# Kernel tuning notes

Measured on AMD Instinct MI355X. Metric: run time of the kernel, lower is better.

## Reference

```python
import jax, jax.numpy as jnp
import numpy as np

NUM_HEADS = 16
D_MODEL = 1024
D_K = D_MODEL // NUM_HEADS
B, S = 2, 2048


def setup_inputs() -> dict:
    key = jax.random.key(0)
    ks = jax.random.split(key, 10)
    q = jax.random.normal(ks[0], (B, S, D_MODEL), dtype=jnp.float32)
    k = jax.random.normal(ks[1], (B, S, D_MODEL), dtype=jnp.float32)
    v = jax.random.normal(ks[2], (B, S, D_MODEL), dtype=jnp.float32)
    # causal mask, 1 = keep, 0 = masked (masked_fill(mask==0, -1e9))
    mask = jnp.tril(jnp.ones((S, S), dtype=jnp.int32))[None, None, :, :]
    # Linear weights ~ N(0, 0.02); biases left at torch default-ish small uniform
    std = 0.02
    Wq = jax.random.normal(ks[3], (D_MODEL, D_MODEL), dtype=jnp.float32) * std
    Wk = jax.random.normal(ks[4], (D_MODEL, D_MODEL), dtype=jnp.float32) * std
    Wv = jax.random.normal(ks[5], (D_MODEL, D_MODEL), dtype=jnp.float32) * std
    bound = 1.0 / np.sqrt(D_MODEL)
    bq = jax.random.uniform(ks[6], (D_MODEL,), jnp.float32, -bound, bound)
    bk = jax.random.uniform(ks[7], (D_MODEL,), jnp.float32, -bound, bound)
    bv = jax.random.uniform(ks[8], (D_MODEL,), jnp.float32, -bound, bound)
    return {"q": q, "k": k, "v": v, "mask": mask,
            "Wq": Wq, "bq": bq, "Wk": Wk, "bk": bk, "Wv": Wv, "bv": bv}


def reference(q, k, v, mask, Wq, bq, Wk, bk, Wv, bv):
    # projections (torch Linear: x @ W.T + b), split heads -> [B, H, S, Dk]
    def proj(x, W, b):
        y = x @ W.T + b
        return y.reshape(B, S, NUM_HEADS, D_K).transpose(0, 2, 1, 3)

    qh, kh, vh = proj(q, Wq, bq), proj(k, Wk, bk), proj(v, Wv, bv)
    scores = jnp.einsum('bhqd,bhkd->bhqk', qh, kh) / jnp.sqrt(jnp.float32(D_K))
    scores = jnp.where(mask == 0, jnp.float32(-1e9), scores)
    p = jax.nn.softmax(scores, axis=-1)
    # dropout is identity in eval mode
    x = jnp.einsum('bhqk,bhkd->bhqd', p, vh)  # [B, H, S, Dk]
    return x.transpose(0, 2, 1, 3).reshape(B, S, D_MODEL)
```

## Files before the change

kernel.cpp:

```cpp
#include <hip/hip_runtime.h>

#define B_ 2
#define H_ 16
#define S_ 2048
#define DM 1024
#define DK 64
#define NX (4096 * 1024)
#define NW (1024 * 1024)

typedef unsigned short u16;
typedef __attribute__((ext_vector_type(8))) short bf16x8;
typedef __attribute__((ext_vector_type(8))) unsigned short u16x8;
typedef __attribute__((ext_vector_type(4))) unsigned short u16x4;
typedef __attribute__((ext_vector_type(4))) float f32x4;

__device__ inline u16 f2bf(float f) {
  union { float f; unsigned int u; } c; c.f = f;
  unsigned int u = c.u;
  u += 0x7fffu + ((u >> 16) & 1u);
  return (u16)(u >> 16);
}

__device__ inline u16x8 cvt8(const float* __restrict__ src) {
  const float4 a = *reinterpret_cast<const float4*>(src);
  const float4 b = *reinterpret_cast<const float4*>(src + 4);
  u16x8 r;
  r[0] = f2bf(a.x); r[1] = f2bf(a.y); r[2] = f2bf(a.z); r[3] = f2bf(a.w);
  r[4] = f2bf(b.x); r[5] = f2bf(b.y); r[6] = f2bf(b.z); r[7] = f2bf(b.w);
  return r;
}

__device__ inline void glds16(const u16* g, u16* l) {
  __builtin_amdgcn_global_load_lds(
      (const __attribute__((address_space(1))) unsigned int*)g,
      (__attribute__((address_space(3))) unsigned int*)l, 16, 0, 0);
}

__global__ __launch_bounds__(256) void cvt_kernel(
    const float* __restrict__ q, const float* __restrict__ k, const float* __restrict__ v,
    const float* __restrict__ Wq, const float* __restrict__ Wk, const float* __restrict__ Wv,
    u16* __restrict__ Xq, u16* __restrict__ Xk, u16* __restrict__ Xv,
    u16* __restrict__ Wqb, u16* __restrict__ Wkb, u16* __restrict__ Wvb)
{
  const int t = blockIdx.y;
  const float* src = (t == 0) ? q : (t == 1) ? k : (t == 2) ? v
                   : (t == 3) ? Wq : (t == 4) ? Wk : Wv;
  u16* dst = (t == 0) ? Xq : (t == 1) ? Xk : (t == 2) ? Xv
           : (t == 3) ? Wqb : (t == 4) ? Wkb : Wvb;
  const int n = (t < 3) ? NX : NW;
  const int idx = (blockIdx.x * 256 + threadIdx.x) * 8;
  if (idx >= n) return;
  *reinterpret_cast<u16x8*>(&dst[idx]) = cvt8(&src[idx]);
}

__global__ __launch_bounds__(256) void proj_kernel(
    const u16* __restrict__ Xq, const u16* __restrict__ Xk, const u16* __restrict__ Xv,
    const u16* __restrict__ Wqb, const u16* __restrict__ Wkb, const u16* __restrict__ Wvb,
    const float* __restrict__ bq, const float* __restrict__ bk, const float* __restrict__ bv,
    u16* __restrict__ Qh, u16* __restrict__ Kh, u16* __restrict__ Vh)
{
  const int z = blockIdx.z;
  const u16* X      = (z == 0) ? Xq : (z == 1) ? Xk : Xv;
  const u16* W      = (z == 0) ? Wqb : (z == 1) ? Wkb : Wvb;
  const float* bias = (z == 0) ? bq : (z == 1) ? bk : bv;
  u16* out          = (z == 0) ? Qh : (z == 1) ? Kh : Vh;
  const float scale = (z == 0) ? 0.125f : 1.0f;

  __shared__ __align__(16) u16 Xs[128 * 32];
  __shared__ __align__(16) u16 Ws[128 * 32];

  const int tid = threadIdx.x;
  const int lane = tid & 63;
  const int w = tid >> 6;
  const int wy = w >> 1, wx = w & 1;
  const int m0 = blockIdx.y * 128;
  const int n0 = blockIdx.x * 128;
  const int ml = lane & 15;
  const int qd = lane >> 4;

  f32x4 acc[4][4] = {};

  for (int kb = 0; kb < DM; kb += 32) {
    __syncthreads();
    #pragma unroll
    for (int p = 0; p < 2; ++p) {
      const int c = p * 4 + w;
      const int row = c * 16 + (lane >> 2);
      const int col = kb + (lane & 3) * 8;
      glds16(&X[(size_t)(m0 + row) * DM + col], &Xs[c * 512]);
      glds16(&W[(size_t)(n0 + row) * DM + col], &Ws[c * 512]);
    }
    __syncthreads();
    bf16x8 a[4], bfr[4];
    #pragma unroll
    for (int i = 0; i < 4; ++i)
      a[i] = *reinterpret_cast<const bf16x8*>(&Xs[(wy * 64 + i * 16 + ml) * 32 + qd * 8]);
    #pragma unroll
    for (int j = 0; j < 4; ++j)
      bfr[j] = *reinterpret_cast<const bf16x8*>(&Ws[(wx * 64 + j * 16 + ml) * 32 + qd * 8]);
    #pragma unroll
    for (int i = 0; i < 4; ++i)
      #pragma unroll
      for (int j = 0; j < 4; ++j)
        acc[i][j] = __builtin_amdgcn_mfma_f32_16x16x32_bf16(a[i], bfr[j], acc[i][j], 0, 0, 0);
  }

  #pragma unroll
  for (int j = 0; j < 4; ++j) {
    const int n = n0 + wx * 64 + j * 16 + ml;
    const float badd = bias[n];
    const int h = n >> 6, d = n & 63;
    #pragma unroll
    for (int i = 0; i < 4; ++i) {
      #pragma unroll
      for (int r = 0; r < 4; ++r) {
        const int m = m0 + wy * 64 + i * 16 + qd * 4 + r;
        const int bi = m >> 11, s = m & 2047;
        out[((bi * H_ + h) * S_ + s) * DK + d] = f2bf((acc[i][j][r] + badd) * scale);
      }
    }
  }
}

__global__ __launch_bounds__(256) void transpose_kernel(
    const u16* __restrict__ Vh, u16* __restrict__ Vt)
{
  __shared__ __align__(16) u16 T[64 * 72];
  const int t = threadIdx.x;
  const int st = blockIdx.x, bh = blockIdx.y;
  {
    const int r = t >> 2, c = (t & 3) * 16;
    const u16* src = &Vh[((size_t)bh * S_ + st * 64 + r) * DK + c];
    *reinterpret_cast<u16x8*>(&T[r * 72 + c])     = *reinterpret_cast<const u16x8*>(src);
    *reinterpret_cast<u16x8*>(&T[r * 72 + c + 8]) = *reinterpret_cast<const u16x8*>(src + 8);
  }
  __syncthreads();
  {
    const int d = t >> 2, s0 = (t & 3) * 16;
    u16x8 a, b;
    #pragma unroll
    for (int i = 0; i < 8; ++i) a[i] = T[(s0 + i) * 72 + d];
    #pragma unroll
    for (int i = 0; i < 8; ++i) b[i] = T[(s0 + 8 + i) * 72 + d];
    u16* dst = &Vt[((size_t)bh * DK + d) * S_ + st * 64 + s0];
    *reinterpret_cast<u16x8*>(dst)     = a;
    *reinterpret_cast<u16x8*>(dst + 8) = b;
  }
}

__global__ __launch_bounds__(256) void attn_kernel(
    const u16* __restrict__ Qh, const u16* __restrict__ Kh,
    const u16* __restrict__ Vt, float* __restrict__ out)
{
  __shared__ __align__(16) u16 Ks[64 * 72];
  __shared__ __align__(16) u16 Vs[64 * 72];
  __shared__ __align__(16) u16 Ps[4 * 16 * 72];

  const int tid  = threadIdx.x;
  const int lane = tid & 63;
  const int w    = tid >> 6;
  const int qt   = (gridDim.x - 1) - blockIdx.x;
  const int bh   = blockIdx.y;
  const int b    = bh >> 4, h = bh & 15;
  const int ml   = lane & 15, qd = lane >> 4;
  const int R0   = qt * 64 + w * 16;

  bf16x8 qa[2];
  #pragma unroll
  for (int ch = 0; ch < 2; ++ch)
    qa[ch] = *reinterpret_cast<const bf16x8*>(
        &Qh[((size_t)bh * S_ + R0 + ml) * DK + ch * 32 + qd * 8]);

  f32x4 oacc[4] = {};
  float l = 0.f;

  const u16* kbase = Kh + (size_t)bh * S_ * DK;
  const u16* vbase = Vt + (size_t)bh * DK * S_;
  u16* pw = &Ps[w * 16 * 72 + ml * 72];

  const int sr = tid >> 3;
  const int sc = (tid & 7) * 8;

  for (int t = 0; t <= qt; ++t) {
    __syncthreads();
    #pragma unroll
    for (int p = 0; p < 2; ++p) {
      const int r = sr + p * 32;
      *reinterpret_cast<float4*>(&Ks[r * 72 + sc]) =
          *reinterpret_cast<const float4*>(&kbase[(size_t)(t * 64 + r) * DK + sc]);
      *reinterpret_cast<float4*>(&Vs[r * 72 + sc]) =
          *reinterpret_cast<const float4*>(&vbase[(size_t)r * S_ + t * 64 + sc]);
    }
    __syncthreads();

    const bool diag = (t == qt);
    const int jmax = diag ? w : 3;

    f32x4 sfr[4];
    #pragma unroll
    for (int j = 0; j < 4; ++j) {
      if (j > jmax) break;
      f32x4 zz = {};
      #pragma unroll
      for (int ch = 0; ch < 2; ++ch) {
        bf16x8 kb = *reinterpret_cast<const bf16x8*>(&Ks[(j * 16 + ml) * 72 + ch * 32 + qd * 8]);
        zz = __builtin_amdgcn_mfma_f32_16x16x32_bf16(kb, qa[ch], zz, 0, 0, 0);
      }
      sfr[j] = zz;
    }

    if (diag) {
      #pragma unroll
      for (int r = 0; r < 4; ++r)
        if (qd * 4 + r > ml) sfr[jmax][r] = -1e30f;
    }

    #pragma unroll
    for (int j = 0; j < 4; ++j) {
      if (j <= jmax) {
        u16x4 pk;
        #pragma unroll
        for (int r = 0; r < 4; ++r) {
          const float e = __expf(sfr[j][r]);
          l += e;
          pk[r] = f2bf(e);
        }
        *reinterpret_cast<u16x4*>(&pw[j * 16 + qd * 4]) = pk;
      } else {
        *reinterpret_cast<u16x4*>(&pw[j * 16 + qd * 4]) = (u16x4){0, 0, 0, 0};
      }
    }

    const int chmax = (diag && w < 2) ? 0 : 1;
    #pragma unroll
    for (int ch = 0; ch < 2; ++ch) {
      if (ch > chmax) break;
      bf16x8 pa = *reinterpret_cast<const bf16x8*>(&Ps[w * 16 * 72 + ml * 72 + ch * 32 + qd * 8]);
      #pragma unroll
      for (int dj = 0; dj < 4; ++dj) {
        bf16x8 vb = *reinterpret_cast<const bf16x8*>(&Vs[(dj * 16 + ml) * 72 + ch * 32 + qd * 8]);
        oacc[dj] = __builtin_amdgcn_mfma_f32_16x16x32_bf16(pa, vb, oacc[dj], 0, 0, 0);
      }
    }
  }

  l += __shfl_xor(l, 16, 64);
  l += __shfl_xor(l, 32, 64);
  float lr[4];
  #pragma unroll
  for (int r = 0; r < 4; ++r) lr[r] = __shfl(l, qd * 4 + r, 64);
  #pragma unroll
  for (int dj = 0; dj < 4; ++dj)
    #pragma unroll
    for (int r = 0; r < 4; ++r) {
      const int srow = R0 + qd * 4 + r;
      out[(size_t)(b * S_ + srow) * DM + h * DK + dj * 16 + ml] = oacc[dj][r] / lr[r];
    }
}

extern "C" void kernel_launch(void* const* d_in, const int* in_sizes, int n_in,
                              void* d_out, int out_size, void* d_ws, size_t ws_size,
                              hipStream_t stream) {
  const float* q  = (const float*)d_in[0];
  const float* k  = (const float*)d_in[1];
  const float* v  = (const float*)d_in[2];
  const float* Wq = (const float*)d_in[4];
  const float* bq = (const float*)d_in[5];
  const float* Wk = (const float*)d_in[6];
  const float* bk = (const float*)d_in[7];
  const float* Wv = (const float*)d_in[8];
  const float* bv = (const float*)d_in[9];

  u16* Xq  = (u16*)d_ws;
  u16* Xk  = Xq + NX;
  u16* Xv  = Xk + NX;
  u16* Wqb = Xv + NX;
  u16* Wkb = Wqb + NW;
  u16* Wvb = Wkb + NW;
  u16* Qh  = Wvb + NW;
  u16* Kh  = Qh + NX;
  u16* Vh  = Kh + NX;
  u16* Vt  = Xq;

  cvt_kernel<<<dim3(NX / (256 * 8), 6), 256, 0, stream>>>(
      q, k, v, Wq, Wk, Wv, Xq, Xk, Xv, Wqb, Wkb, Wvb);
  proj_kernel<<<dim3(DM / 128, (B_ * S_) / 128, 3), 256, 0, stream>>>(
      Xq, Xk, Xv, Wqb, Wkb, Wvb, bq, bk, bv, Qh, Kh, Vh);
  transpose_kernel<<<dim3(S_ / 64, B_ * H_), 256, 0, stream>>>(Vh, Vt);
  attn_kernel<<<dim3(S_ / 64, B_ * H_), 256, 0, stream>>>(
      Qh, Kh, Vt, (float*)d_out);
}
```

Measured before the change: 234.5 us.

## Split attention KV range across two blocks, merge partials, prefetch K/V tiles

The attention grid gains a z dimension that splits each query tile's causal KV range in half. Each half writes unnormalized bf16 partial outputs and row sums to workspace, and a new merge kernel combines them and normalizes. The change also prefetches the next K/V tile into registers, switches to exp2 with log2(e) folded into the Q scale, packs bf16 values with perm, and doubles the projection GEMM K-tile to 64. It aims to balance causal work and raise occupancy, at the cost of an extra kernel, extra global traffic and bf16 rounding of the partials.

```diff
diff --git a/kernel.cpp b/kernel.cpp
--- a/kernel.cpp
+++ b/kernel.cpp
@@ -7,18 +7,23 @@
 #define DK 64
 #define NX (4096 * 1024)
 #define NW (1024 * 1024)
+#define NO (32 * 2048 * 64)
 
 typedef unsigned short u16;
+typedef unsigned int u32;
 typedef __attribute__((ext_vector_type(8))) short bf16x8;
 typedef __attribute__((ext_vector_type(8))) unsigned short u16x8;
-typedef __attribute__((ext_vector_type(4))) unsigned short u16x4;
 typedef __attribute__((ext_vector_type(4))) float f32x4;
 
 __device__ inline u16 f2bf(float f) {
-  union { float f; unsigned int u; } c; c.f = f;
-  unsigned int u = c.u;
+  union { float f; u32 u; } c; c.f = f;
+  u32 u = c.u;
   u += 0x7fffu + ((u >> 16) & 1u);
   return (u16)(u >> 16);
+}
+__device__ inline float bf2f(u16 v) {
+  union { u32 u; float f; } c; c.u = ((u32)v) << 16;
+  return c.f;
 }
 
 __device__ inline u16x8 cvt8(const float* __restrict__ src) {
@@ -64,10 +69,10 @@
   const u16* W      = (z == 0) ? Wqb : (z == 1) ? Wkb : Wvb;
   const float* bias = (z == 0) ? bq : (z == 1) ? bk : bv;
   u16* out          = (z == 0) ? Qh : (z == 1) ? Kh : Vh;
-  const float scale = (z == 0) ? 0.125f : 1.0f;
-
-  __shared__ __align__(16) u16 Xs[128 * 32];
-  __shared__ __align__(16) u16 Ws[128 * 32];
+  const float scale = (z == 0) ? 0.18033688f : 1.0f;
+
+  __shared__ __align__(16) u16 Xs[128 * 64];
+  __shared__ __align__(16) u16 Ws[128 * 64];
 
   const int tid = threadIdx.x;
   const int lane = tid & 63;
@@ -80,29 +85,35 @@
 
   f32x4 acc[4][4] = {};
 
-  for (int kb = 0; kb < DM; kb += 32) {
+  for (int kb = 0; kb < DM; kb += 64) {
     __syncthreads();
     #pragma unroll
-    for (int p = 0; p < 2; ++p) {
+    for (int p = 0; p < 4; ++p) {
       const int c = p * 4 + w;
-      const int row = c * 16 + (lane >> 2);
-      const int col = kb + (lane & 3) * 8;
+      const int row = c * 8 + (lane >> 3);
+      const int col = kb + (lane & 7) * 8;
       glds16(&X[(size_t)(m0 + row) * DM + col], &Xs[c * 512]);
       glds16(&W[(size_t)(n0 + row) * DM + col], &Ws[c * 512]);
     }
     __syncthreads();
-    bf16x8 a[4], bfr[4];
+    bf16x8 a[4][2], bfr[4][2];
     #pragma unroll
     for (int i = 0; i < 4; ++i)
-      a[i] = *reinterpret_cast<const bf16x8*>(&Xs[(wy * 64 + i * 16 + ml) * 32 + qd * 8]);
+      #pragma unroll
+      for (int kc = 0; kc < 2; ++kc)
+        a[i][kc] = *reinterpret_cast<const bf16x8*>(&Xs[(wy * 64 + i * 16 + ml) * 64 + kc * 32 + qd * 8]);
     #pragma unroll
     for (int j = 0; j < 4; ++j)
-      bfr[j] = *reinterpret_cast<const bf16x8*>(&Ws[(wx * 64 + j * 16 + ml) * 32 + qd * 8]);
+      #pragma unroll
+      for (int kc = 0; kc < 2; ++kc)
+        bfr[j][kc] = *reinterpret_cast<const bf16x8*>(&Ws[(wx * 64 + j * 16 + ml) * 64 + kc * 32 + qd * 8]);
     #pragma unroll
     for (int i = 0; i < 4; ++i)
       #pragma unroll
-      for (int j = 0; j < 4; ++j)
-        acc[i][j] = __builtin_amdgcn_mfma_f32_16x16x32_bf16(a[i], bfr[j], acc[i][j], 0, 0, 0);
+      for (int j = 0; j < 4; ++j) {
+        acc[i][j] = __builtin_amdgcn_mfma_f32_16x16x32_bf16(a[i][0], bfr[j][0], acc[i][j], 0, 0, 0);
+        acc[i][j] = __builtin_amdgcn_mfma_f32_16x16x32_bf16(a[i][1], bfr[j][1], acc[i][j], 0, 0, 0);
+      }
   }
 
   #pragma unroll
@@ -150,7 +161,7 @@
 
 __global__ __launch_bounds__(256) void attn_kernel(
     const u16* __restrict__ Qh, const u16* __restrict__ Kh,
-    const u16* __restrict__ Vt, float* __restrict__ out)
+    const u16* __restrict__ Vt, u16* __restrict__ Op, float* __restrict__ lp)
 {
   __shared__ __align__(16) u16 Ks[64 * 72];
   __shared__ __align__(16) u16 Vs[64 * 72];
@@ -159,9 +170,13 @@
   const int tid  = threadIdx.x;
   const int lane = tid & 63;
   const int w    = tid >> 6;
-  const int qt   = (gridDim.x - 1) - blockIdx.x;
+  const int qt   = 31 - blockIdx.x;
   const int bh   = blockIdx.y;
-  const int b    = bh >> 4, h = bh & 15;
+  const int half = blockIdx.z;
+  const int nt   = qt + 1;
+  const int na   = (nt + 1) >> 1;
+  const int t0   = half ? na : 0;
+  const int t1   = half ? nt : na;
   const int ml   = lane & 15, qd = lane >> 4;
   const int R0   = qt * 64 + w * 16;
 
@@ -181,17 +196,26 @@
   const int sr = tid >> 3;
   const int sc = (tid & 7) * 8;
 
-  for (int t = 0; t <= qt; ++t) {
+  float4 kr0 = *reinterpret_cast<const float4*>(&kbase[(size_t)(t0 * 64 + sr) * DK + sc]);
+  float4 kr1 = *reinterpret_cast<const float4*>(&kbase[(size_t)(t0 * 64 + sr + 32) * DK + sc]);
+  float4 vr0 = *reinterpret_cast<const float4*>(&vbase[(size_t)sr * S_ + t0 * 64 + sc]);
+  float4 vr1 = *reinterpret_cast<const float4*>(&vbase[(size_t)(sr + 32) * S_ + t0 * 64 + sc]);
+
+  for (int t = t0; t < t1; ++t) {
     __syncthreads();
-    #pragma unroll
-    for (int p = 0; p < 2; ++p) {
-      const int r = sr + p * 32;
-      *reinterpret_cast<float4*>(&Ks[r * 72 + sc]) =
-          *reinterpret_cast<const float4*>(&kbase[(size_t)(t * 64 + r) * DK + sc]);
-      *reinterpret_cast<float4*>(&Vs[r * 72 + sc]) =
-          *reinterpret_cast<const float4*>(&vbase[(size_t)r * S_ + t * 64 + sc]);
-    }
+    *reinterpret_cast<float4*>(&Ks[sr * 72 + sc])        = kr0;
+    *reinterpret_cast<float4*>(&Ks[(sr + 32) * 72 + sc]) = kr1;
+    *reinterpret_cast<float4*>(&Vs[sr * 72 + sc])        = vr0;
+    *reinterpret_cast<float4*>(&Vs[(sr + 32) * 72 + sc]) = vr1;
     __syncthreads();
+
+    if (t + 1 < t1) {
+      const int tn = t + 1;
+      kr0 = *reinterpret_cast<const float4*>(&kbase[(size_t)(tn * 64 + sr) * DK + sc]);
+      kr1 = *reinterpret_cast<const float4*>(&kbase[(size_t)(tn * 64 + sr + 32) * DK + sc]);
+      vr0 = *reinterpret_cast<const float4*>(&vbase[(size_t)sr * S_ + tn * 64 + sc]);
+      vr1 = *reinterpret_cast<const float4*>(&vbase[(size_t)(sr + 32) * S_ + tn * 64 + sc]);
+    }
 
     const bool diag = (t == qt);
     const int jmax = diag ? w : 3;
@@ -217,18 +241,19 @@
 
     #pragma unroll
     for (int j = 0; j < 4; ++j) {
+      u32 p0 = 0, p1 = 0;
       if (j <= jmax) {
-        u16x4 pk;
-        #pragma unroll
-        for (int r = 0; r < 4; ++r) {
-          const float e = __expf(sfr[j][r]);
-          l += e;
-          pk[r] = f2bf(e);
-        }
-        *reinterpret_cast<u16x4*>(&pw[j * 16 + qd * 4]) = pk;
-      } else {
-        *reinterpret_cast<u16x4*>(&pw[j * 16 + qd * 4]) = (u16x4){0, 0, 0, 0};
-      }
+        union { float f; u32 u; } e0, e1, e2, e3;
+        e0.f = __builtin_amdgcn_exp2f(sfr[j][0]);
+        e1.f = __builtin_amdgcn_exp2f(sfr[j][1]);
+        e2.f = __builtin_amdgcn_exp2f(sfr[j][2]);
+        e3.f = __builtin_amdgcn_exp2f(sfr[j][3]);
+        l += (e0.f + e1.f) + (e2.f + e3.f);
+        p0 = __builtin_amdgcn_perm(e1.u, e0.u, 0x07060302u);
+        p1 = __builtin_amdgcn_perm(e3.u, e2.u, 0x07060302u);
+      }
+      u32* pd = reinterpret_cast<u32*>(&pw[j * 16 + qd * 4]);
+      pd[0] = p0; pd[1] = p1;
     }
 
     const int chmax = (diag && w < 2) ? 0 : 1;
@@ -246,16 +271,39 @@
 
   l += __shfl_xor(l, 16, 64);
   l += __shfl_xor(l, 32, 64);
-  float lr[4];
-  #pragma unroll
-  for (int r = 0; r < 4; ++r) lr[r] = __shfl(l, qd * 4 + r, 64);
+  const size_t rbase = (size_t)(half * 32 + bh) * S_;
+  if (qd == 0) lp[rbase + R0 + ml] = l;
   #pragma unroll
   for (int dj = 0; dj < 4; ++dj)
     #pragma unroll
-    for (int r = 0; r < 4; ++r) {
-      const int srow = R0 + qd * 4 + r;
-      out[(size_t)(b * S_ + srow) * DM + h * DK + dj * 16 + ml] = oacc[dj][r] / lr[r];
-    }
+    for (int r = 0; r < 4; ++r)
+      Op[(rbase + R0 + qd * 4 + r) * DK + dj * 16 + ml] = f2bf(oacc[dj][r]);
+}
+
+__global__ __launch_bounds__(256) void merge_kernel(
+    const u16* __restrict__ Op, const float* __restrict__ lp,
+    float* __restrict__ out)
+{
+  const int idx8 = (blockIdx.x * 256 + threadIdx.x) * 8;
+  const int row = idx8 >> 6;
+  const int d = idx8 & 63;
+  const float inv = 1.f / (lp[row] + lp[row + 32 * S_]);
+  const u16x8 a = *reinterpret_cast<const u16x8*>(&Op[idx8]);
+  const u16x8 c = *reinterpret_cast<const u16x8*>(&Op[(size_t)idx8 + NO]);
+  const int bh = row >> 11, s = row & 2047;
+  const int b = bh >> 4, h = bh & 15;
+  float* dst = &out[(size_t)(b * S_ + s) * DM + h * DK + d];
+  float4 o0, o1;
+  o0.x = (bf2f(a[0]) + bf2f(c[0])) * inv;
+  o0.y = (bf2f(a[1]) + bf2f(c[1])) * inv;
+  o0.z = (bf2f(a[2]) + bf2f(c[2])) * inv;
+  o0.w = (bf2f(a[3]) + bf2f(c[3])) * inv;
+  o1.x = (bf2f(a[4]) + bf2f(c[4])) * inv;
+  o1.y = (bf2f(a[5]) + bf2f(c[5])) * inv;
+  o1.z = (bf2f(a[6]) + bf2f(c[6])) * inv;
+  o1.w = (bf2f(a[7]) + bf2f(c[7])) * inv;
+  *reinterpret_cast<float4*>(dst)     = o0;
+  *reinterpret_cast<float4*>(dst + 4) = o1;
 }
 
 extern "C" void kernel_launch(void* const* d_in, const int* in_sizes, int n_in,
@@ -281,12 +329,15 @@
   u16* Kh  = Qh + NX;
   u16* Vh  = Kh + NX;
   u16* Vt  = Xq;
+  u16* Op  = Xk;
+  float* lp = (float*)Wqb;
 
   cvt_kernel<<<dim3(NX / (256 * 8), 6), 256, 0, stream>>>(
       q, k, v, Wq, Wk, Wv, Xq, Xk, Xv, Wqb, Wkb, Wvb);
   proj_kernel<<<dim3(DM / 128, (B_ * S_) / 128, 3), 256, 0, stream>>>(
       Xq, Xk, Xv, Wqb, Wkb, Wvb, bq, bk, bv, Qh, Kh, Vh);
   transpose_kernel<<<dim3(S_ / 64, B_ * H_), 256, 0, stream>>>(Vh, Vt);
-  attn_kernel<<<dim3(S_ / 64, B_ * H_), 256, 0, stream>>>(
-      Qh, Kh, Vt, (float*)d_out);
-}
+  attn_kernel<<<dim3(32, B_ * H_, 2), 256, 0, stream>>>(
+      Qh, Kh, Vt, Op, lp);
+  merge_kernel<<<NO / (256 * 8), 256, 0, stream>>>(Op, lp, (float*)d_out);
+}
```

New measurement: 245.8 us. +4.8%, slower.
